# Kernel tuning notes

Hardware: AMD Instinct MI355X
Metric: run time of the kernel (lower is better)

Reference implementation:

```python
import jax, jax.numpy as jnp
import numpy as np

N_UNITS = 100
N_INPUTS = 7
N_OUTPUTS = 1
T = 60
STIM_ON, STIM_OFF = 10, 15
RESP_START, RESP_END = 20, 35
REWARD_DURATION = 5
ALPHA = 0.2            # dt / tau = 100 / 500
SIGMA_REC = 0.15
B = 8192


def setup_inputs() -> dict:
    key = jax.random.key(0)
    k1, k2, k3, k4, k5, k6, k7 = jax.random.split(key, 7)
    W_in_raw = (jax.random.normal(k1, (N_UNITS, N_INPUTS)) * 0.05).astype(jnp.float32)
    W_rec_np = np.asarray(jax.random.normal(k2, (N_UNITS, N_UNITS))) / np.sqrt(N_UNITS)
    sr = float(np.abs(np.linalg.eigvals(W_rec_np)).max())
    W_rec = jnp.asarray(W_rec_np * (0.8 / sr), dtype=jnp.float32)
    b_rec = jnp.zeros((N_UNITS,), jnp.float32)
    w_out = (jax.random.normal(k3, (N_OUTPUTS, N_UNITS)) * 0.1).astype(jnp.float32)
    b_out = jnp.zeros((N_OUTPUTS,), jnp.float32)
    return {
        "y0": jnp.zeros((B, N_UNITS), jnp.float32),
        "noise": jax.random.normal(k4, (B, T, N_UNITS), dtype=jnp.float32),
        "stimulus_idx": jax.random.randint(k5, (B,), 0, 4).astype(jnp.int32),
        "rewarded_target_idx": jax.random.randint(k6, (B,), 0, 4).astype(jnp.int32),
        "instruction": jax.random.randint(k7, (B,), 0, 2).astype(jnp.int32),
        "W_in_raw": W_in_raw, "W_rec": W_rec, "b_rec": b_rec,
        "w_out": w_out, "b_out": b_out,
    }


def reference(y0, noise, stimulus_idx, rewarded_target_idx, instruction,
              W_in_raw, W_rec, b_rec, w_out, b_out):
    W_in = jnp.abs(W_in_raw)               # [N, n_in]
    w_lick = W_in[:, 5]
    w_reward = W_in[:, 4]
    noise_scale = SIGMA_REC * float(np.sqrt(2.0 * ALPHA))
    t_idx = jnp.arange(T, dtype=jnp.int32)
    stim_mask = ((t_idx >= STIM_ON) & (t_idx < STIM_OFF)).astype(jnp.float32)
    resp_mask = ((t_idx >= RESP_START) & (t_idx < RESP_END)).astype(jnp.float32)
    auto_start = RESP_END - REWARD_DURATION

    def trial(y0_i, eps_i, stim, rew, instr):
        is_rew = stim == rew
        instr_b = instr > 0
        # base open-loop input: stimulus channel + response cue (channel 6)
        u_base = jnp.zeros((T, N_INPUTS), jnp.float32).at[:, 6].set(resp_mask)
        u_base = u_base + stim_mask[:, None] * jax.nn.one_hot(stim, N_INPUTS, dtype=jnp.float32)
        wu = u_base @ W_in.T + b_rec        # [T, N]

        def step(carry, xs):
            y, licked, lick_t, instr_fired = carry
            t, wu_t, eps_t = xs
            # instruction auto-reward fires at auto_start if no reward yet (applied BEFORE pre)
            delivered = instr_fired | (licked & is_rew)
            fire = instr_b & (~delivered) & (t == auto_start)
            instr_fired = instr_fired | fire
            instr_active = instr_fired & (t >= auto_start) & (t < RESP_END)
            # lick-triggered inputs affect dynamics only AFTER the lick step (wu[t] already consumed)
            lick_dyn = licked & (t > lick_t) & (t < lick_t + REWARD_DURATION)
            add = (instr_active.astype(jnp.float32) + (lick_dyn & is_rew).astype(jnp.float32)) * w_reward \
                  + lick_dyn.astype(jnp.float32) * w_lick
            pre = y @ W_rec.T + wu_t + add + noise_scale * eps_t
            y = (1.0 - ALPHA) * y + ALPHA * jax.nn.relu(pre)
            z = jax.nn.sigmoid(y @ w_out.T + b_out)[0]
            # closed-loop lick decision (after readout)
            in_resp = (t >= RESP_START) & (t < RESP_END)
            trig = in_resp & (~licked) & (z > 0.5)
            lick_t = jnp.where(trig, t, lick_t)
            licked = licked | trig
            # u_trial markings include the lick step itself
            u5 = licked & (t >= lick_t) & (t < lick_t + REWARD_DURATION)
            u4 = instr_active | (u5 & is_rew)
            return (y, licked, lick_t, instr_fired), (z, u5, u4)

        init = (y0_i, jnp.array(False), jnp.array(T + 1, jnp.int32), jnp.array(False))
        (yf, licked, lick_t, instr_fired), (z_seq, u5, u4) = jax.lax.scan(
            step, init, (t_idx, wu, eps_i))
        u = u_base.at[:, 5].set(u5.astype(jnp.float32)).at[:, 4].set(u4.astype(jnp.float32))
        reward_delivered = instr_fired | (licked & is_rew)
        target = jnp.where(is_rew, resp_mask, jnp.zeros_like(resp_mask))
        return u, target, resp_mask > 0, licked, reward_delivered, z_seq, yf

    return jax.vmap(trial)(y0, noise, stimulus_idx, rewarded_target_idx, instruction)
```

## Files before the change

### kernel.cpp

```cpp
#include <hip/hip_runtime.h>
#include <math.h>

#define BB 8192
#define TT 60
#define NU 100
#define NI 7

#define L32A(M) M(0) M(1) M(2) M(3) M(4) M(5) M(6) M(7) M(8) M(9) M(10) M(11) \
  M(12) M(13) M(14) M(15) M(16) M(17) M(18) M(19) M(20) M(21) M(22) M(23) \
  M(24) M(25) M(26) M(27) M(28) M(29) M(30) M(31)
#define L32B(M) M(32) M(33) M(34) M(35) M(36) M(37) M(38) M(39) M(40) M(41) \
  M(42) M(43) M(44) M(45) M(46) M(47) M(48) M(49) M(50) M(51) M(52) M(53) \
  M(54) M(55) M(56) M(57) M(58) M(59) M(60) M(61) M(62) M(63)
#define P36(M) M(64,0) M(65,1) M(66,2) M(67,3) M(68,4) M(69,5) M(70,6) \
  M(71,7) M(72,8) M(73,9) M(74,10) M(75,11) M(76,12) M(77,13) M(78,14) \
  M(79,15) M(80,16) M(81,17) M(82,18) M(83,19) M(84,20) M(85,21) M(86,22) \
  M(87,23) M(88,24) M(89,25) M(90,26) M(91,27) M(92,28) M(93,29) M(94,30) \
  M(95,31) M(96,32) M(97,33) M(98,34) M(99,35)

#define DW(k)    const float w1_##k = W_rec[u1o + k]; const float w2_##k = W_rec[u2o + k];
#define DW2(k,j) DW(k)

#define RL(v,l) __int_as_float(__builtin_amdgcn_readlane(__float_as_int(v), l))
#define MACA(k)   { const float yk = RL(y1, k);  pre1 += yk * w1_##k; pre2 += yk * w2_##k; }
#define MACB(k)   { const float yk = RL(y1, k);  p1b  += yk * w1_##k; p2b  += yk * w2_##k; }
#define MACC(k,j) { const float yk = RL(y2, j);  pre1 += yk * w1_##k; pre2 += yk * w2_##k; }

__global__ __launch_bounds__(256, 2)
void drr_kernel(const float* __restrict__ y0,
                const float* __restrict__ noise,
                const int*   __restrict__ stim_idx,
                const int*   __restrict__ rew_idx,
                const int*   __restrict__ instr_in,
                const float* __restrict__ W_in_raw,
                const float* __restrict__ W_rec,
                const float* __restrict__ b_rec,
                const float* __restrict__ w_out,
                const float* __restrict__ b_out,
                float* __restrict__ out)
{
    const int lane  = threadIdx.x & 63;
    const int wid   = threadIdx.x >> 6;
    const int trial = blockIdx.x * 4 + wid;

    const int  u1   = lane;
    const int  u2   = 64 + lane;
    const bool has2 = (u2 < NU);
    const int  u2c  = has2 ? u2 : (NU - 1);

    const int u1o = u1  * NU;
    const int u2o = u2c * NU;

    const int  stim    = stim_idx[trial];
    const int  rew     = rew_idx[trial];
    const bool is_rew  = (stim == rew);
    const bool instr_b = (instr_in[trial] > 0);

    L32A(DW) L32B(DW) P36(DW2)

    const float wi6_1 = fabsf(W_in_raw[u1  * NI + 6]);
    const float wis_1 = fabsf(W_in_raw[u1  * NI + stim]);
    const float wr_1  = fabsf(W_in_raw[u1  * NI + 4]);
    const float wl_1  = fabsf(W_in_raw[u1  * NI + 5]);
    const float wi6_2 = fabsf(W_in_raw[u2c * NI + 6]);
    const float wis_2 = fabsf(W_in_raw[u2c * NI + stim]);
    const float wr_2  = fabsf(W_in_raw[u2c * NI + 4]);
    const float wl_2  = fabsf(W_in_raw[u2c * NI + 5]);

    const float br_1 = b_rec[u1];
    const float br_2 = b_rec[u2c];
    const float wo_1 = w_out[u1];
    const float wo_2 = has2 ? w_out[u2] : 0.0f;
    const float bo   = b_out[0];

    float y1 = y0[trial * NU + u1];
    float y2 = has2 ? y0[trial * NU + u2] : 0.0f;

    const float NS = 0.09486832980505138f;

    bool licked = false, instr_fired = false;
    int  lick_t = TT + 1;

    const int nbase = trial * (TT * NU);
    float e1n = noise[nbase + u1];
    float e2n = noise[nbase + u2c];

    float* uout  = out;
    float* tout  = out  + BB * TT * NI;
    float* rout  = tout + BB * TT;
    float* lout  = rout + BB * TT;
    float* dout  = lout + BB;
    float* zout  = dout + BB;
    float* yfout = zout + BB * TT;

    for (int t = 0; t < TT; ++t) {
        const float e1 = e1n, e2 = e2n;
        if (t < TT - 1) {
            e1n = noise[nbase + (t + 1) * NU + u1];
            e2n = noise[nbase + (t + 1) * NU + u2c];
        }

        const float sm = (t >= 10 && t < 15) ? 1.0f : 0.0f;
        const float rm = (t >= 20 && t < 35) ? 1.0f : 0.0f;

        const bool delivered    = instr_fired || (licked && is_rew);
        const bool fire         = instr_b && !delivered && (t == 30);
        instr_fired             = instr_fired || fire;
        const bool instr_active = instr_fired && (t >= 30) && (t < 35);
        const bool lick_dyn     = licked && (t > lick_t) && (t < lick_t + 5);
        const float a_rew  = (instr_active ? 1.0f : 0.0f) + ((lick_dyn && is_rew) ? 1.0f : 0.0f);
        const float a_lick = lick_dyn ? 1.0f : 0.0f;

        float pre1 = br_1 + rm * wi6_1 + sm * wis_1 + a_rew * wr_1 + a_lick * wl_1 + NS * e1;
        float pre2 = br_2 + rm * wi6_2 + sm * wis_2 + a_rew * wr_2 + a_lick * wl_2 + NS * e2;
        float p1b = 0.0f, p2b = 0.0f;

        L32A(MACA)
        L32B(MACB)
        P36(MACC)

        pre1 += p1b;
        pre2 += p2b;

        y1 = 0.8f * y1 + 0.2f * fmaxf(pre1, 0.0f);
        y2 = 0.8f * y2 + 0.2f * fmaxf(pre2, 0.0f);

        float part = y1 * wo_1 + y2 * wo_2;
        #pragma unroll
        for (int off = 32; off >= 1; off >>= 1)
            part += __shfl_xor(part, off);
        const float x = part + bo;
        const float z = 1.0f / (1.0f + expf(-x));

        const bool in_resp = (t >= 20) && (t < 35);
        const bool trig    = in_resp && !licked && (z > 0.5f);
        if (trig) lick_t = t;
        licked = licked || trig;
        const bool u5 = licked && (t >= lick_t) && (t < lick_t + 5);
        const bool u4 = instr_active || (u5 && is_rew);

        const int bt = trial * TT + t;
        if (lane < NI) {
            float uv = 0.0f;
            if (lane == stim) uv = sm;
            if (lane == 4)    uv = u4 ? 1.0f : 0.0f;
            if (lane == 5)    uv = u5 ? 1.0f : 0.0f;
            if (lane == 6)    uv = rm;
            uout[bt * NI + lane] = uv;
        } else if (lane == 8) {
            tout[bt] = is_rew ? rm : 0.0f;
        } else if (lane == 9) {
            rout[bt] = rm;
        } else if (lane == 10) {
            zout[bt] = z;
        }
    }

    if (lane == 0) {
        lout[trial] = licked ? 1.0f : 0.0f;
        dout[trial] = (instr_fired || (licked && is_rew)) ? 1.0f : 0.0f;
    }
    yfout[trial * NU + u1] = y1;
    if (has2) yfout[trial * NU + u2] = y2;
}

extern "C" void kernel_launch(void* const* d_in, const int* in_sizes, int n_in,
                              void* d_out, int out_size, void* d_ws, size_t ws_size,
                              hipStream_t stream) {
    const float* y0       = (const float*)d_in[0];
    const float* noise    = (const float*)d_in[1];
    const int*   stim     = (const int*)  d_in[2];
    const int*   rew      = (const int*)  d_in[3];
    const int*   instr    = (const int*)  d_in[4];
    const float* W_in_raw = (const float*)d_in[5];
    const float* W_rec    = (const float*)d_in[6];
    const float* b_rec    = (const float*)d_in[7];
    const float* w_out    = (const float*)d_in[8];
    const float* b_out    = (const float*)d_in[9];
    float* out = (float*)d_out;

    drr_kernel<<<BB / 4, 256, 0, stream>>>(y0, noise, stim, rew, instr,
                                           W_in_raw, W_rec, b_rec, w_out, b_out, out);
}
```

Measured before the change: 620.7 us.

## Pack two adjacent units per lane and use packed float2 FMAs

Remaps the recurrent matvec so each of 50 active lanes owns two adjacent units (2k, 2k+1) held in a float2, rather than units lane and lane+64. The inner loop does 50 readlane pairs and packed v2f multiply-adds, with four accumulators to split dependency chains, aiming to cut the readlane count and use packed FP32 math. Noise, y0 and the final state move as 8-byte vector accesses. The trade-off is 14 idle lanes per wavefront and a possible change in register pressure from the packed weight layout.

New measurement: 619.3 us. About the same (-0.2%).

```diff
diff --git a/kernel.cpp b/kernel.cpp
--- a/kernel.cpp
+++ b/kernel.cpp
@@ -6,25 +6,25 @@
 #define NU 100
 #define NI 7
 
-#define L32A(M) M(0) M(1) M(2) M(3) M(4) M(5) M(6) M(7) M(8) M(9) M(10) M(11) \
-  M(12) M(13) M(14) M(15) M(16) M(17) M(18) M(19) M(20) M(21) M(22) M(23) \
-  M(24) M(25) M(26) M(27) M(28) M(29) M(30) M(31)
-#define L32B(M) M(32) M(33) M(34) M(35) M(36) M(37) M(38) M(39) M(40) M(41) \
-  M(42) M(43) M(44) M(45) M(46) M(47) M(48) M(49) M(50) M(51) M(52) M(53) \
-  M(54) M(55) M(56) M(57) M(58) M(59) M(60) M(61) M(62) M(63)
-#define P36(M) M(64,0) M(65,1) M(66,2) M(67,3) M(68,4) M(69,5) M(70,6) \
-  M(71,7) M(72,8) M(73,9) M(74,10) M(75,11) M(76,12) M(77,13) M(78,14) \
-  M(79,15) M(80,16) M(81,17) M(82,18) M(83,19) M(84,20) M(85,21) M(86,22) \
-  M(87,23) M(88,24) M(89,25) M(90,26) M(91,27) M(92,28) M(93,29) M(94,30) \
-  M(95,31) M(96,32) M(97,33) M(98,34) M(99,35)
+typedef float v2f __attribute__((ext_vector_type(2)));
 
-#define DW(k)    const float w1_##k = W_rec[u1o + k]; const float w2_##k = W_rec[u2o + k];
-#define DW2(k,j) DW(k)
+#define FOR50(M) M(0) M(1) M(2) M(3) M(4) M(5) M(6) M(7) M(8) M(9) \
+  M(10) M(11) M(12) M(13) M(14) M(15) M(16) M(17) M(18) M(19) \
+  M(20) M(21) M(22) M(23) M(24) M(25) M(26) M(27) M(28) M(29) \
+  M(30) M(31) M(32) M(33) M(34) M(35) M(36) M(37) M(38) M(39) \
+  M(40) M(41) M(42) M(43) M(44) M(45) M(46) M(47) M(48) M(49)
+
+#define DECLW(sl) \
+  const v2f wA_##sl = { W_rec[uao + 2*(sl)],     W_rec[ubo + 2*(sl)]     }; \
+  const v2f wB_##sl = { W_rec[uao + 2*(sl) + 1], W_rec[ubo + 2*(sl) + 1] };
 
 #define RL(v,l) __int_as_float(__builtin_amdgcn_readlane(__float_as_int(v), l))
-#define MACA(k)   { const float yk = RL(y1, k);  pre1 += yk * w1_##k; pre2 += yk * w2_##k; }
-#define MACB(k)   { const float yk = RL(y1, k);  p1b  += yk * w1_##k; p2b  += yk * w2_##k; }
-#define MACC(k,j) { const float yk = RL(y2, j);  pre1 += yk * w1_##k; pre2 += yk * w2_##k; }
+
+#define MAC(sl) { \
+  const float ya = RL(yy.x, sl); \
+  const float yb = RL(yy.y, sl); \
+  if ((sl) & 1) { accB0 += ya * wA_##sl; accB1 += yb * wB_##sl; } \
+  else          { accA0 += ya * wA_##sl; accA1 += yb * wB_##sl; } }
 
 __global__ __launch_bounds__(256, 2)
 void drr_kernel(const float* __restrict__ y0,
@@ -43,47 +43,37 @@
     const int wid   = threadIdx.x >> 6;
     const int trial = blockIdx.x * 4 + wid;
 
-    const int  u1   = lane;
-    const int  u2   = 64 + lane;
-    const bool has2 = (u2 < NU);
-    const int  u2c  = has2 ? u2 : (NU - 1);
-
-    const int u1o = u1  * NU;
-    const int u2o = u2c * NU;
+    const bool act = (lane < 50);
+    const int  la  = act ? lane : 49;
+    const int  ua  = 2 * la;
+    const int  uao = ua * NU;
+    const int  ubo = uao + NU;
 
     const int  stim    = stim_idx[trial];
     const int  rew     = rew_idx[trial];
     const bool is_rew  = (stim == rew);
     const bool instr_b = (instr_in[trial] > 0);
 
-    L32A(DW) L32B(DW) P36(DW2)
+    FOR50(DECLW)
 
-    const float wi6_1 = fabsf(W_in_raw[u1  * NI + 6]);
-    const float wis_1 = fabsf(W_in_raw[u1  * NI + stim]);
-    const float wr_1  = fabsf(W_in_raw[u1  * NI + 4]);
-    const float wl_1  = fabsf(W_in_raw[u1  * NI + 5]);
-    const float wi6_2 = fabsf(W_in_raw[u2c * NI + 6]);
-    const float wis_2 = fabsf(W_in_raw[u2c * NI + stim]);
-    const float wr_2  = fabsf(W_in_raw[u2c * NI + 4]);
-    const float wl_2  = fabsf(W_in_raw[u2c * NI + 5]);
+    const v2f wi6 = { fabsf(W_in_raw[ua * NI + 6]),    fabsf(W_in_raw[(ua+1) * NI + 6]) };
+    const v2f wis = { fabsf(W_in_raw[ua * NI + stim]), fabsf(W_in_raw[(ua+1) * NI + stim]) };
+    const v2f wr  = { fabsf(W_in_raw[ua * NI + 4]),    fabsf(W_in_raw[(ua+1) * NI + 4]) };
+    const v2f wl  = { fabsf(W_in_raw[ua * NI + 5]),    fabsf(W_in_raw[(ua+1) * NI + 5]) };
+    const v2f br  = { b_rec[ua], b_rec[ua + 1] };
+    const v2f wo  = act ? (v2f){ w_out[ua], w_out[ua + 1] } : (v2f){ 0.0f, 0.0f };
+    const float bo = b_out[0];
 
-    const float br_1 = b_rec[u1];
-    const float br_2 = b_rec[u2c];
-    const float wo_1 = w_out[u1];
-    const float wo_2 = has2 ? w_out[u2] : 0.0f;
-    const float bo   = b_out[0];
-
-    float y1 = y0[trial * NU + u1];
-    float y2 = has2 ? y0[trial * NU + u2] : 0.0f;
+    const v2f* y0v = (const v2f*)(y0 + trial * NU);
+    v2f yy = y0v[la];
 
     const float NS = 0.09486832980505138f;
 
     bool licked = false, instr_fired = false;
     int  lick_t = TT + 1;
 
-    const int nbase = trial * (TT * NU);
-    float e1n = noise[nbase + u1];
-    float e2n = noise[nbase + u2c];
+    const float* nbase = noise + trial * (TT * NU);
+    v2f en = ((const v2f*)nbase)[la];
 
     float* uout  = out;
     float* tout  = out  + BB * TT * NI;
@@ -94,11 +84,9 @@
     float* yfout = zout + BB * TT;
 
     for (int t = 0; t < TT; ++t) {
-        const float e1 = e1n, e2 = e2n;
-        if (t < TT - 1) {
-            e1n = noise[nbase + (t + 1) * NU + u1];
-            e2n = noise[nbase + (t + 1) * NU + u2c];
-        }
+        const v2f e = en;
+        if (t < TT - 1)
+            en = ((const v2f*)(nbase + (t + 1) * NU))[la];
 
         const float sm = (t >= 10 && t < 15) ? 1.0f : 0.0f;
         const float rm = (t >= 20 && t < 35) ? 1.0f : 0.0f;
@@ -111,21 +99,18 @@
         const float a_rew  = (instr_active ? 1.0f : 0.0f) + ((lick_dyn && is_rew) ? 1.0f : 0.0f);
         const float a_lick = lick_dyn ? 1.0f : 0.0f;
 
-        float pre1 = br_1 + rm * wi6_1 + sm * wis_1 + a_rew * wr_1 + a_lick * wl_1 + NS * e1;
-        float pre2 = br_2 + rm * wi6_2 + sm * wis_2 + a_rew * wr_2 + a_lick * wl_2 + NS * e2;
-        float p1b = 0.0f, p2b = 0.0f;
+        v2f accA0 = br + rm * wi6 + sm * wis + a_rew * wr + a_lick * wl + NS * e;
+        v2f accA1 = { 0.0f, 0.0f };
+        v2f accB0 = { 0.0f, 0.0f };
+        v2f accB1 = { 0.0f, 0.0f };
 
-        L32A(MACA)
-        L32B(MACB)
-        P36(MACC)
+        FOR50(MAC)
 
-        pre1 += p1b;
-        pre2 += p2b;
+        const v2f pre = (accA0 + accA1) + (accB0 + accB1);
+        const v2f prer = { fmaxf(pre.x, 0.0f), fmaxf(pre.y, 0.0f) };
+        yy = 0.8f * yy + 0.2f * prer;
 
-        y1 = 0.8f * y1 + 0.2f * fmaxf(pre1, 0.0f);
-        y2 = 0.8f * y2 + 0.2f * fmaxf(pre2, 0.0f);
-
-        float part = y1 * wo_1 + y2 * wo_2;
+        float part = yy.x * wo.x + yy.y * wo.y;
         #pragma unroll
         for (int off = 32; off >= 1; off >>= 1)
             part += __shfl_xor(part, off);
@@ -160,8 +145,8 @@
         lout[trial] = licked ? 1.0f : 0.0f;
         dout[trial] = (instr_fired || (licked && is_rew)) ? 1.0f : 0.0f;
     }
-    yfout[trial * NU + u1] = y1;
-    if (has2) yfout[trial * NU + u2] = y2;
+    if (act)
+        ((v2f*)(yfout + trial * NU))[la] = yy;
 }
 
 extern "C" void kernel_launch(void* const* d_in, const int* in_sizes, int n_in,
```
